# Performance work log

Measured on AMD Instinct MI355X. Metric: run time of the kernel, lower is better.

The kernel has to match this reference:

```python
import math
import jax, jax.numpy as jnp
from jax import lax
import numpy as np

SCORE_THR = 0.5
IOU_THR = 0.7
MIN_SIZE = 1.0
BBOX_CLIP = math.log(1000.0 / 16.0)

FEAT_SIZES = [100, 50, 25, 13, 7]
STRIDES = [8, 16, 32, 64, 128]
RATIOS = (0.5, 1.0, 2.0)
C = 256
A = 3
N = 2


def _make_priors(fs, stride):
    base = stride * 4.0
    ys, xs = np.meshgrid(np.arange(fs), np.arange(fs), indexing='ij')
    cx = (xs + 0.5) * stride
    cy = (ys + 0.5) * stride
    pri = []
    for r in RATIOS:
        w = base / np.sqrt(r)
        h = base * np.sqrt(r)
        pri.append(np.stack([cx - w / 2, cy - h / 2, cx + w / 2, cy + h / 2], axis=-1))
    pri = np.stack(pri, axis=2)  # (fs, fs, A, 4): H,W,A order matches permute/reshape
    return jnp.asarray(pri.reshape(-1, 4), dtype=jnp.float32)


def setup_inputs():
    key = jax.random.key(0)
    ks = jax.random.split(key, 8)
    inp = {}
    for i, fs in enumerate(FEAT_SIZES):
        inp[f'fmap{i}'] = jax.random.normal(jax.random.fold_in(ks[0], i), (N, C, fs, fs), dtype=jnp.float32)
        inp[f'priors{i}'] = _make_priors(fs, STRIDES[i])
    sc = 0.02
    inp['conv_w'] = jax.random.normal(ks[1], (C, C, 3, 3), jnp.float32) * sc
    inp['conv_b'] = jnp.zeros((C,), jnp.float32)
    inp['log_w'] = jax.random.normal(ks[2], (A, C, 1, 1), jnp.float32) * sc
    inp['log_b'] = jnp.zeros((A,), jnp.float32)
    inp['reg_w'] = jax.random.normal(ks[3], (A * 4, C, 1, 1), jnp.float32) * sc
    inp['reg_b'] = jnp.zeros((A * 4,), jnp.float32)
    inp['imsizes'] = jnp.full((N, 2), 800, dtype=jnp.int32)  # (h, w) per image
    inp['lvtop'] = 500
    inp['imtop'] = 100
    return inp


def _conv(x, w, b, pad):
    y = lax.conv_general_dilated(x, w, (1, 1), pad, dimension_numbers=('NCHW', 'OIHW', 'NCHW'))
    return y + b[None, :, None, None]


def _decode(reg, pri):
    pw = pri[..., 2] - pri[..., 0]
    ph = pri[..., 3] - pri[..., 1]
    pcx = pri[..., 0] + 0.5 * pw
    pcy = pri[..., 1] + 0.5 * ph
    dx, dy = reg[..., 0], reg[..., 1]
    dw = jnp.minimum(reg[..., 2], BBOX_CLIP)
    dh = jnp.minimum(reg[..., 3], BBOX_CLIP)
    cx = dx * pw + pcx
    cy = dy * ph + pcy
    w = jnp.exp(dw) * pw
    h = jnp.exp(dh) * ph
    return jnp.stack([cx - 0.5 * w, cy - 0.5 * h, cx + 0.5 * w, cy + 0.5 * h], axis=-1)


def _head(x, priors, conv_w, conv_b, log_w, log_b, reg_w, reg_b, lvtop):
    n = x.shape[0]
    h = jax.nn.relu(_conv(x, conv_w, conv_b, 'SAME'))
    reg = _conv(h, reg_w, reg_b, 'VALID').transpose(0, 2, 3, 1).reshape(n, -1, 4)
    log = _conv(h, log_w, log_b, 'VALID').transpose(0, 2, 3, 1).reshape(n, -1)
    k = min(lvtop, log.shape[1])
    vals, top = lax.top_k(log, k)                           # (n, k)
    reg = jnp.take_along_axis(reg, top[..., None], axis=1)  # (n, k, 4)
    pri = priors[top]                                       # (n, k, 4)
    return _decode(reg, pri), vals, k


def _box_iou(a, b):
    area_a = (a[:, 2] - a[:, 0]) * (a[:, 3] - a[:, 1])
    area_b = (b[:, 2] - b[:, 0]) * (b[:, 3] - b[:, 1])
    lt = jnp.maximum(a[:, None, :2], b[None, :, :2])
    rb = jnp.minimum(a[:, None, 2:], b[None, :, 2:])
    wh = jnp.clip(rb - lt, 0.0)
    inter = wh[..., 0] * wh[..., 1]
    return inter / (area_a[:, None] + area_b[None, :] - inter + 1e-9)


def _forward(fmaps, priors, conv_w, conv_b, log_w, log_b, reg_w, reg_b, imsizes, lvtop, imtop):
    tups = [_head(x, p, conv_w, conv_b, log_w, log_b, reg_w, reg_b, lvtop)
            for x, p in zip(fmaps, priors)]
    boxes = jnp.concatenate([t[0] for t in tups], axis=1)                 # (n, D, 4)
    obj = jax.nn.sigmoid(jnp.concatenate([t[1] for t in tups], axis=1))   # (n, D)
    lvlen = jnp.asarray([t[2] for t in tups])
    n, D = obj.shape
    boxes = boxes.reshape(-1, 4)
    obj = obj.reshape(-1)
    K = n * D
    imidx = jnp.arange(K) // D
    valid = obj >= SCORE_THR                                # score filter (masked, not nonzero)
    hw = imsizes[imidx].astype(jnp.float32)                 # (K, 2) = (h, w)
    x1 = jnp.clip(boxes[:, 0], 0.0, hw[:, 1])
    y1 = jnp.clip(boxes[:, 1], 0.0, hw[:, 0])
    x2 = jnp.clip(boxes[:, 2], 0.0, hw[:, 1])
    y2 = jnp.clip(boxes[:, 3], 0.0, hw[:, 0])
    boxes = jnp.stack([x1, y1, x2, y2], axis=-1)
    valid &= (x2 - x1 >= MIN_SIZE) & (y2 - y1 >= MIN_SIZE)  # remove_small
    lvidx = jnp.searchsorted(jnp.cumsum(lvlen), jnp.arange(K) % D, side='right')
    groups = imidx * 10 + lvidx
    scores = jnp.where(valid, obj, -jnp.inf)
    order = jnp.argsort(-scores)                            # global score order; groups gate suppression
    b, g, v, ii = boxes[order], groups[order], valid[order], imidx[order]
    iou = _box_iou(b, b)                                    # (K, K)
    ar = jnp.arange(K)
    def body(i, keep):
        sup = (iou[i] > IOU_THR) & (g == g[i]) & (ar > i)
        return jnp.where(keep[i], keep & ~sup, keep)
    keep = lax.fori_loop(0, K, body, v)                     # greedy batched NMS
    def select(i):
        m = keep & (ii == i)
        sel = jnp.argsort(~m)[:imtop]                       # stable: kept boxes in score order
        val = m[sel]
        bx = jnp.where(val[:, None], b[sel], 0.0)
        ix = jnp.where(val, i, -1)
        return bx, ix
    bx, ix = jax.vmap(select)(jnp.arange(n))
    return bx.reshape(n * imtop, 4), ix.reshape(n * imtop)


def reference(fmap0, fmap1, fmap2, fmap3, fmap4, priors0, priors1, priors2, priors3, priors4,
              conv_w, conv_b, log_w, log_b, reg_w, reg_b, imsizes, lvtop, imtop):
    return _forward([fmap0, fmap1, fmap2, fmap3, fmap4],
                    [priors0, priors1, priors2, priors3, priors4],
                    conv_w, conv_b, log_w, log_b, reg_w, reg_b, imsizes, lvtop, imtop)
```

## Files before the change

### kernel.cpp

```cpp
#include <hip/hip_runtime.h>
#include <math.h>


#define N_IMG 2
#define C_CH  256
#define D_PER 2147
#define K_TOT 4294
#define K_PAD 8192

__constant__ int c_Ml[5]     = {30000, 7500, 1875, 507, 147};
__constant__ int c_kl[5]     = {500, 500, 500, 500, 147};
__constant__ int c_lvoff[5]  = {0, 500, 1000, 1500, 2000};
__constant__ int c_logoff[5] = {0, 60000, 75000, 78750, 79764};
__constant__ int c_regoff[5] = {0, 240000, 300000, 315000, 319056};
__constant__ int c_fs[5]     = {100, 50, 25, 13, 7};
__constant__ int c_npt[5]    = {13, 7, 4, 2, 1};
__constant__ int c_E[5]      = {10000, 2500, 625, 169, 49};
__constant__ int c_cumbl[6]  = {0, 1352, 1744, 1872, 1904, 1912};
__constant__ int c_hcum[6]   = {0, 157, 197, 207, 210, 211};
__constant__ size_t c_hoff[5] = {0, 5120000, 6400000, 6720000, 6806528};

__global__ void transpose_w_kernel(const float* __restrict__ w,
                                   double* __restrict__ wT2) {
  int i = blockIdx.x * 256 + threadIdx.x;
  if (i >= 589824) return;
  int q = i % 4608;
  int slab = i / 4608;
  int cobi = slab >> 5, ch = slab & 31;
  int ci = q / 576;
  int rem = q % 576;
  int tap = rem / 64, co = rem & 63;
  wT2[i] = (double)w[(size_t)(cobi * 64 + co) * 2304 + (ch * 8 + ci) * 9 + tap];
}

template <typename T>
__global__ __launch_bounds__(256) void conv_fused_kernel(
    const float* __restrict__ x0, const float* __restrict__ x1,
    const float* __restrict__ x2, const float* __restrict__ x3,
    const float* __restrict__ x4, const double* __restrict__ wT2,
    const float* __restrict__ bias, T* __restrict__ h) {
  __shared__ double s_in[8][120];
  __shared__ double s_w[4608];
  int tid = threadIdx.x;
  int bid = blockIdx.x;
  int l = 0;
  while (bid >= c_cumbl[l + 1]) ++l;
  int r = bid - c_cumbl[l];
  int fs = c_fs[l], npt = c_npt[l];
  int tiles = npt * npt;
  int tile = r % tiles;
  int cn = r / tiles;
  int cobi = cn & 3, n = cn >> 2;
  int ptx = tile % npt, pty = tile / npt;
  int px0 = ptx * 8, py0 = pty * 8;
  int E = fs * fs;
  const float* xl;
  switch (l) {
    case 0: xl = x0; break;
    case 1: xl = x1; break;
    case 2: xl = x2; break;
    case 3: xl = x3; break;
    default: xl = x4; break;
  }
  const float* xn = xl + (size_t)n * C_CH * E;
  T* hl = h + c_hoff[l];

  int tpx = tid & 15, tco = tid >> 4;
  int prow = tpx >> 1, pcol0 = (tpx & 1) * 4;

  double acc[4][4];
#pragma unroll
  for (int i = 0; i < 4; i++)
#pragma unroll
    for (int j = 0; j < 4; j++) acc[i][j] = 0.0;

  for (int ch = 0; ch < 32; ++ch) {
    for (int idx = tid; idx < 800; idx += 256) {
      int ci = idx / 100, rr2 = idx % 100;
      int hy = rr2 / 10, hx = rr2 % 10;
      int gy = py0 - 1 + hy, gx = px0 - 1 + hx;
      float v = 0.f;
      if (gy >= 0 && gy < fs && gx >= 0 && gx < fs)
        v = xn[(size_t)(ch * 8 + ci) * E + gy * fs + gx];
      s_in[ci][hy * 12 + hx] = (double)v;
    }
    {
      const double2* src =
          (const double2*)(wT2 + (size_t)(cobi * 32 + ch) * 4608);
      double2* dst = (double2*)s_w;
#pragma unroll
      for (int k = 0; k < 9; k++) {
        int idx = tid + k * 256;
        if (idx < 2304) dst[idx] = src[idx];
      }
    }
    __syncthreads();
#pragma unroll
    for (int ci = 0; ci < 8; ++ci) {
      const double* inp = &s_in[ci][0];
      const double* wpb = &s_w[ci * 576];
#pragma unroll
      for (int ky = 0; ky < 3; ++ky) {
        const double* ip = inp + (prow + ky) * 12 + pcol0;
        double2 a0 = *(const double2*)ip;
        double2 a1 = *(const double2*)(ip + 2);
        double2 a2 = *(const double2*)(ip + 4);
        double d6[6];
        d6[0] = a0.x; d6[1] = a0.y; d6[2] = a1.x;
        d6[3] = a1.y; d6[4] = a2.x; d6[5] = a2.y;
#pragma unroll
        for (int kx = 0; kx < 3; ++kx) {
          const double* wp = wpb + (ky * 3 + kx) * 64 + tco * 4;
          double2 wA = *(const double2*)wp;
          double2 wB = *(const double2*)(wp + 2);
          double w0 = wA.x, w1 = wA.y, w2 = wB.x, w3 = wB.y;
#pragma unroll
          for (int pj = 0; pj < 4; pj++) {
            double iv = d6[pj + kx];
            acc[0][pj] = fma(w0, iv, acc[0][pj]);
            acc[1][pj] = fma(w1, iv, acc[1][pj]);
            acc[2][pj] = fma(w2, iv, acc[2][pj]);
            acc[3][pj] = fma(w3, iv, acc[3][pj]);
          }
        }
      }
    }
    __syncthreads();
  }

  int gy = py0 + prow;
  if (gy < fs) {
#pragma unroll
    for (int coi = 0; coi < 4; ++coi) {
      int co = cobi * 64 + tco * 4 + coi;
      double bb = (double)bias[co];
#pragma unroll
      for (int pj = 0; pj < 4; pj++) {
        int gx = px0 + pcol0 + pj;
        if (gx < fs) {
          double v = acc[coi][pj] + bb;
          hl[((size_t)n * C_CH + co) * E + gy * fs + gx] = (T)fmax(v, 0.0);
        }
      }
    }
  }
}

template <typename T>
__global__ __launch_bounds__(256) void heads_fused_kernel(
    const T* __restrict__ h, const float* __restrict__ logw,
    const float* __restrict__ logb, const float* __restrict__ regw,
    const float* __restrict__ regb, double* __restrict__ logits,
    double* __restrict__ regs) {
  __shared__ float s_wh[256][16];
  __shared__ double s_red[4][15][64];
  int tid = threadIdx.x;
  int n = blockIdx.y;
  int cidx = blockIdx.x;
  int l = 0;
  while (cidx >= c_hcum[l + 1]) ++l;
  int chunk = cidx - c_hcum[l];
  int E = c_E[l];
  int px0 = chunk * 64;
  const T* hl = h + c_hoff[l];
  double* logits_l = logits + c_logoff[l];
  double* regs_l = regs + c_regoff[l];

  for (int idx = tid; idx < 4096; idx += 256) {
    int c = idx >> 4, j = idx & 15;
    float v = 0.f;
    if (j < 3) v = logw[j * 256 + c];
    else if (j < 15) v = regw[(j - 3) * 256 + c];
    s_wh[c][j] = v;
  }
  __syncthreads();

  int p = tid & 63, c4 = tid >> 6;
  int pix = px0 + p;
  bool act = pix < E;
  double acc[15];
#pragma unroll
  for (int j = 0; j < 15; j++) acc[j] = 0.0;
  if (act) {
    const T* hp = hl + ((size_t)n * C_CH + c4 * 64) * E + pix;
    for (int cc = 0; cc < 64; ++cc) {
      double hv = (double)hp[(size_t)cc * E];
      const float* wr = &s_wh[c4 * 64 + cc][0];
#pragma unroll
      for (int j = 0; j < 15; j++)
        acc[j] = fma((double)wr[j], hv, acc[j]);
    }
  }
#pragma unroll
  for (int j = 0; j < 15; j++) s_red[c4][j][p] = acc[j];
  __syncthreads();
  if (act) {
    int M = E * 3;
    for (int j = c4; j < 15; j += 4) {
      double v = s_red[0][j][p] + s_red[1][j][p] + s_red[2][j][p] +
                 s_red[3][j][p];
      if (j < 3) {
        logits_l[(size_t)n * M + pix * 3 + j] = v + (double)logb[j];
      } else {
        int rj = j - 3, a = rj >> 2, coord = rj & 3;
        regs_l[((size_t)n * M + pix * 3 + a) * 4 + coord] =
            v + (double)regb[rj];
      }
    }
  }
}

__device__ __forceinline__ unsigned long long d2key(double v) {
  unsigned long long ub = (unsigned long long)__double_as_longlong(v);
  return (ub >> 63) ? ~ub : (ub | 0x8000000000000000ull);
}

#define TK_CH 30
__global__ __launch_bounds__(1024) void topk_kernel(
    const double* __restrict__ logits, int* __restrict__ cand_anchor) {
  int bid = blockIdx.x;
  int n = bid / 5, l = bid % 5;
  int M = c_Ml[l], k = c_kl[l];
  const double* lg = logits + c_logoff[l] + (size_t)n * M;
  int tid = threadIdx.x;
  __shared__ int histw[16][256];
  __shared__ int hist[256];
  __shared__ unsigned long long s_prefix;
  __shared__ int s_r;
  if (tid == 0) { s_prefix = 0ull; s_r = k; }

  int chunk = (M + 1023) >> 10;
  int i0 = tid * chunk, i1 = min(M, i0 + chunk);
  int cnt = i1 - i0;
  if (cnt < 0) cnt = 0;
  unsigned long long kv[TK_CH];
#pragma unroll
  for (int q = 0; q < TK_CH; q++)
    if (q < cnt) kv[q] = d2key(lg[i0 + q]);
  int wid = tid >> 6;
  __syncthreads();

  for (int pass = 0; pass < 8; ++pass) {
    int shift = 56 - pass * 8;
    for (int i = tid; i < 4096; i += 1024) ((int*)histw)[i] = 0;
    __syncthreads();
    unsigned long long pfx = s_prefix;
    int rr = s_r;
#pragma unroll
    for (int q = 0; q < TK_CH; q++) {
      if (q < cnt) {
        unsigned long long u = kv[q];
        if (pass == 0 || (u >> (shift + 8)) == pfx)
          atomicAdd(&histw[wid][(int)((u >> shift) & 255ull)], 1);
      }
    }
    __syncthreads();
    if (tid < 256) {
      int s = 0;
#pragma unroll
      for (int w = 0; w < 16; w++) s += histw[w][tid];
      hist[tid] = s;
    }
    __syncthreads();
    if (tid == 0) {
      int s = 0, beta = 0;
      for (int b = 255; b >= 0; --b) {
        if (s + hist[b] >= rr) { beta = b; break; }
        s += hist[b];
      }
      s_prefix = (pfx << 8) | (unsigned long long)beta;
      s_r = rr - s;
    }
    __syncthreads();
  }
  unsigned long long T = s_prefix;
  int need = s_r;
  int cgt = 0, ceq = 0;
#pragma unroll
  for (int q = 0; q < TK_CH; q++) {
    if (q < cnt) {
      cgt += (kv[q] > T);
      ceq += (kv[q] == T);
    }
  }
  __shared__ int sgt[1024], seq[1024];
  sgt[tid] = cgt;
  seq[tid] = ceq;
  __syncthreads();
  for (int o = 1; o < 1024; o <<= 1) {
    int a = (tid >= o) ? sgt[tid - o] : 0;
    int b2 = (tid >= o) ? seq[tid - o] : 0;
    __syncthreads();
    sgt[tid] += a;
    seq[tid] += b2;
    __syncthreads();
  }
  int gt_total = sgt[1023];
  int pg = sgt[tid] - cgt, pe = seq[tid] - ceq;
  int base = n * D_PER + c_lvoff[l];
#pragma unroll
  for (int q = 0; q < TK_CH; q++) {
    if (q < cnt) {
      unsigned long long u = kv[q];
      if (u > T) {
        cand_anchor[base + (pg++)] = i0 + q;
      } else if (u == T) {
        if (pe < need) cand_anchor[base + gt_total + pe] = i0 + q;
        pe++;
      }
    }
  }
}

__global__ __launch_bounds__(256) void decode_kernel(
    const int* __restrict__ cand_anchor, const double* __restrict__ logits,
    const double* __restrict__ regs, const float* __restrict__ p0,
    const float* __restrict__ p1, const float* __restrict__ p2,
    const float* __restrict__ p3, const float* __restrict__ p4,
    const int* __restrict__ imsizes, double* __restrict__ cand_score,
    double* __restrict__ cand_box, int* __restrict__ cand_group,
    int* __restrict__ cand_valid) {
  int s = blockIdx.x * 256 + threadIdx.x;
  if (s >= K_TOT) return;
  int n = s / D_PER;
  int rr = s % D_PER;
  int l = (rr < 2000) ? (rr / 500) : 4;
  int aidx = cand_anchor[s];
  int M = c_Ml[l];
  const float* pp;
  switch (l) {
    case 0: pp = p0; break;
    case 1: pp = p1; break;
    case 2: pp = p2; break;
    case 3: pp = p3; break;
    default: pp = p4; break;
  }
  double lv = logits[c_logoff[l] + (size_t)n * M + aidx];
  double obj = 1.0 / (1.0 + exp(-lv));
  const double* rp = regs + c_regoff[l] + ((size_t)n * M + aidx) * 4;
  const float* pr = pp + (size_t)aidx * 4;
  double px1 = pr[0], py1 = pr[1], px2 = pr[2], py2 = pr[3];
  double pw = px2 - px1, ph = py2 - py1;
  double pcx = px1 + 0.5 * pw, pcy = py1 + 0.5 * ph;
  const double BCLIP = 4.1351665567423560;
  double dx = rp[0], dy = rp[1];
  double dw = fmin(rp[2], BCLIP), dh = fmin(rp[3], BCLIP);
  double cx = dx * pw + pcx, cy = dy * ph + pcy;
  double w = exp(dw) * pw, hh = exp(dh) * ph;
  double x1 = cx - 0.5 * w, y1 = cy - 0.5 * hh;
  double x2 = cx + 0.5 * w, y2 = cy + 0.5 * hh;
  double imh = (double)imsizes[n * 2 + 0], imw = (double)imsizes[n * 2 + 1];
  x1 = fmin(fmax(x1, 0.0), imw);
  x2 = fmin(fmax(x2, 0.0), imw);
  y1 = fmin(fmax(y1, 0.0), imh);
  y2 = fmin(fmax(y2, 0.0), imh);
  bool valid = (obj >= 0.5) && ((x2 - x1) >= 1.0) && ((y2 - y1) >= 1.0);
  cand_box[(size_t)s * 4 + 0] = x1;
  cand_box[(size_t)s * 4 + 1] = y1;
  cand_box[(size_t)s * 4 + 2] = x2;
  cand_box[(size_t)s * 4 + 3] = y2;
  cand_score[s] = valid ? obj : -(double)INFINITY;
  cand_group[s] = n * 5 + l;
  cand_valid[s] = valid ? 1 : 0;
}

__global__ __launch_bounds__(1024) void sort_kernel(
    const double* __restrict__ cand_score, int* __restrict__ order) {
  __shared__ unsigned long long key[K_PAD];
  int tid = threadIdx.x;
  for (int i = tid; i < K_PAD; i += 1024) {
    unsigned long long kk = 0ull;
    if (i < K_TOT) {
      unsigned long long u = d2key(cand_score[i]);
      kk = (u & ~0x1FFFull) | (unsigned long long)i;
    }
    key[i] = kk;
  }
  __syncthreads();
  for (int k = 2; k <= K_PAD; k <<= 1) {
    for (int j = k >> 1; j > 0; j >>= 1) {
      for (int i = tid; i < K_PAD; i += 1024) {
        int ixj = i ^ j;
        if (ixj > i) {
          unsigned long long a = key[i], b = key[ixj];
          bool sw = ((i & k) == 0) ? (a < b) : (a > b);
          if (sw) { key[i] = b; key[ixj] = a; }
        }
      }
      __syncthreads();
    }
  }
  for (int i = tid; i < K_TOT; i += 1024)
    order[i] = (int)(key[i] & 0x1FFFull);
}

__global__ __launch_bounds__(256) void gather_kernel(
    const int* __restrict__ order, const double* __restrict__ cand_box,
    const int* __restrict__ cand_group, const int* __restrict__ cand_valid,
    double* __restrict__ box_s, int* __restrict__ grp_s,
    int* __restrict__ img_s, int* __restrict__ valid_s,
    int* __restrict__ keep_s) {
  int i = blockIdx.x * 256 + threadIdx.x;
  if (i >= K_TOT) return;
  int s = order[i];
#pragma unroll
  for (int q = 0; q < 4; q++)
    box_s[(size_t)i * 4 + q] = cand_box[(size_t)s * 4 + q];
  int g = cand_group[s];
  grp_s[i] = g;
  img_s[i] = g / 5;
  valid_s[i] = cand_valid[s];
  keep_s[i] = 0;
}

#define MAXM 512
__global__ __launch_bounds__(256) void nms_kernel(
    const double* __restrict__ box_s, const int* __restrict__ grp_s,
    const int* __restrict__ valid_s, int* __restrict__ keep_s) {
  int g = blockIdx.x;
  int tid = threadIdx.x;
  __shared__ int cnt[256];
  __shared__ int mem[MAXM];
  __shared__ double bx[MAXM][4];
  __shared__ unsigned long long mask[MAXM][8];
  const int chunk = (K_TOT + 255) / 256;
  int i0 = tid * chunk, i1 = min(K_TOT, i0 + chunk);
  int c = 0;
  for (int i = i0; i < i1; ++i) c += (grp_s[i] == g && valid_s[i]);
  cnt[tid] = c;
  __syncthreads();
  for (int o = 1; o < 256; o <<= 1) {
    int v = (tid >= o) ? cnt[tid - o] : 0;
    __syncthreads();
    cnt[tid] += v;
    __syncthreads();
  }
  int off = cnt[tid] - c;
  int m = cnt[255];
  for (int i = i0; i < i1; ++i)
    if (grp_s[i] == g && valid_s[i]) mem[off++] = i;
  __syncthreads();
  for (int t = tid; t < m; t += 256) {
    int i = mem[t];
#pragma unroll
    for (int q = 0; q < 4; q++) bx[t][q] = box_s[(size_t)i * 4 + q];
  }
  __syncthreads();
  for (int i = tid; i < m; i += 256) {
    unsigned long long row[8] = {0, 0, 0, 0, 0, 0, 0, 0};
    double ax1 = bx[i][0], ay1 = bx[i][1], ax2 = bx[i][2], ay2 = bx[i][3];
    double areaA = (ax2 - ax1) * (ay2 - ay1);
    for (int j = i + 1; j < m; ++j) {
      double bx1 = bx[j][0], by1 = bx[j][1], bx2 = bx[j][2], by2 = bx[j][3];
      double areaB = (bx2 - bx1) * (by2 - by1);
      double lx = fmax(ax1, bx1), ly = fmax(ay1, by1);
      double rx = fmin(ax2, bx2), ry = fmin(ay2, by2);
      double iw = fmax(rx - lx, 0.0), ih = fmax(ry - ly, 0.0);
      double inter = iw * ih;
      double iou = inter / (areaA + areaB - inter + 1e-9);
      if (iou > 0.7) row[j >> 6] |= (1ull << (j & 63));
    }
#pragma unroll
    for (int w2 = 0; w2 < 8; ++w2) mask[i][w2] = row[w2];
  }
  __syncthreads();
  if (tid == 0) {
    unsigned long long remv[8] = {0, 0, 0, 0, 0, 0, 0, 0};
    for (int i = 0; i < m; ++i) {
      if (!((remv[i >> 6] >> (i & 63)) & 1ull)) {
        keep_s[mem[i]] = 1;
#pragma unroll
        for (int w2 = 0; w2 < 8; ++w2) remv[w2] |= mask[i][w2];
      }
    }
  }
}

__global__ __launch_bounds__(256) void select_kernel(
    const double* __restrict__ box_s, const int* __restrict__ img_s,
    const int* __restrict__ keep_s, float* __restrict__ out) {
  int n = blockIdx.x;
  int tid = threadIdx.x;
  __shared__ int cnt[256];
  const int chunk = (K_TOT + 255) / 256;
  int i0 = tid * chunk, i1 = min(K_TOT, i0 + chunk);
  int c = 0;
  for (int i = i0; i < i1; ++i) c += (keep_s[i] && img_s[i] == n);
  cnt[tid] = c;
  __syncthreads();
  for (int o = 1; o < 256; o <<= 1) {
    int v = (tid >= o) ? cnt[tid - o] : 0;
    __syncthreads();
    cnt[tid] += v;
    __syncthreads();
  }
  int pos = cnt[tid] - c;
  int total = cnt[255];
  for (int i = i0; i < i1; ++i) {
    if (keep_s[i] && img_s[i] == n) {
      if (pos < 100) {
#pragma unroll
        for (int q = 0; q < 4; q++)
          out[(n * 100 + pos) * 4 + q] = (float)box_s[(size_t)i * 4 + q];
        out[800 + n * 100 + pos] = (float)n;
      }
      pos++;
    }
  }
  for (int p = total + tid; p < 100; p += 256) {
#pragma unroll
    for (int q = 0; q < 4; q++) out[(n * 100 + p) * 4 + q] = 0.0f;
    out[800 + n * 100 + p] = -1.0f;
  }
}

extern "C" void kernel_launch(void* const* d_in, const int* in_sizes, int n_in,
                              void* d_out, int out_size, void* d_ws,
                              size_t ws_size, hipStream_t stream) {
  (void)in_sizes; (void)n_in; (void)out_size;
  const float* fmap[5];
  const float* priors[5];
  for (int l = 0; l < 5; l++) {
    fmap[l] = (const float*)d_in[2 * l];
    priors[l] = (const float*)d_in[2 * l + 1];
  }
  const float* conv_w = (const float*)d_in[10];
  const float* conv_b = (const float*)d_in[11];
  const float* log_w = (const float*)d_in[12];
  const float* log_b = (const float*)d_in[13];
  const float* reg_w = (const float*)d_in[14];
  const float* reg_b = (const float*)d_in[15];
  const int* imsizes = (const int*)d_in[16];
  float* out = (float*)d_out;

  bool f64h = ws_size >= (size_t)66000000;

  char* base = (char*)d_ws;
  size_t off = 0;
  auto alloc = [&](size_t bytes) -> void* {
    off = (off + 255) & ~(size_t)255;
    void* p = base + off;
    off += bytes;
    return p;
  };
  double* wT2 = (double*)alloc(589824ull * 8);
  void* hraw = alloc(6831616ull * (f64h ? 8 : 4));
  double* logits = (double*)alloc(80058ull * 8);
  double* regs = (double*)alloc(320232ull * 8);
  int* cand_anchor = (int*)alloc(K_TOT * 4);
  double* cand_score = (double*)alloc(K_TOT * 8);
  double* cand_box = (double*)alloc((size_t)K_TOT * 4 * 8);
  int* cand_group = (int*)alloc(K_TOT * 4);
  int* cand_valid = (int*)alloc(K_TOT * 4);
  int* order = (int*)alloc(K_TOT * 4);
  double* box_s = (double*)alloc((size_t)K_TOT * 4 * 8);
  int* grp_s = (int*)alloc(K_TOT * 4);
  int* img_s = (int*)alloc(K_TOT * 4);
  int* valid_s = (int*)alloc(K_TOT * 4);
  int* keep_s = (int*)alloc(K_TOT * 4);

  transpose_w_kernel<<<2304, 256, 0, stream>>>(conv_w, wT2);

  if (f64h) {
    conv_fused_kernel<double><<<1912, 256, 0, stream>>>(
        fmap[0], fmap[1], fmap[2], fmap[3], fmap[4], wT2, conv_b,
        (double*)hraw);
    heads_fused_kernel<double><<<dim3(211, 2), 256, 0, stream>>>(
        (double*)hraw, log_w, log_b, reg_w, reg_b, logits, regs);
  } else {
    conv_fused_kernel<float><<<1912, 256, 0, stream>>>(
        fmap[0], fmap[1], fmap[2], fmap[3], fmap[4], wT2, conv_b,
        (float*)hraw);
    heads_fused_kernel<float><<<dim3(211, 2), 256, 0, stream>>>(
        (float*)hraw, log_w, log_b, reg_w, reg_b, logits, regs);
  }
  topk_kernel<<<10, 1024, 0, stream>>>(logits, cand_anchor);
  decode_kernel<<<(K_TOT + 255) / 256, 256, 0, stream>>>(
      cand_anchor, logits, regs, priors[0], priors[1], priors[2], priors[3],
      priors[4], imsizes, cand_score, cand_box, cand_group, cand_valid);
  sort_kernel<<<1, 1024, 0, stream>>>(cand_score, order);
  gather_kernel<<<(K_TOT + 255) / 256, 256, 0, stream>>>(
      order, cand_box, cand_group, cand_valid, box_s, grp_s, img_s, valid_s,
      keep_s);
  nms_kernel<<<10, 256, 0, stream>>>(box_s, grp_s, valid_s, keep_s);
  select_kernel<<<2, 256, 0, stream>>>(box_s, img_s, keep_s, out);
}
```

Before: 1.239 ms.

## Halve conv channel chunk, precompute halo indices, and remap block order

The fp64 3x3 conv now stages 4 input channels per iteration instead of 8, which halves shared memory (s_w 2304 doubles, s_in 480) so more blocks can be resident per CU. The halo load addresses are computed once before the channel loop rather than recomputed with divisions every iteration. Block IDs are permuted with a stride of 239 so neighbouring launched blocks come from different regions of the work list, likely to spread them across XCDs. The trade-off is twice as many loop iterations and barriers, with less work per barrier.

```diff
diff --git a/kernel.cpp b/kernel.cpp
--- a/kernel.cpp
+++ b/kernel.cpp
@@ -7,6 +7,8 @@
 #define D_PER 2147
 #define K_TOT 4294
 #define K_PAD 8192
+#define CONV_BLOCKS 1912
+#define CPX 239
 
 __constant__ int c_Ml[5]     = {30000, 7500, 1875, 507, 147};
 __constant__ int c_kl[5]     = {500, 500, 500, 500, 147};
@@ -24,13 +26,14 @@
                                    double* __restrict__ wT2) {
   int i = blockIdx.x * 256 + threadIdx.x;
   if (i >= 589824) return;
-  int q = i % 4608;
-  int slab = i / 4608;
-  int cobi = slab >> 5, ch = slab & 31;
+  int q = i % 2304;
+  int slab = i / 2304;
+  int cobi = slab >> 6, ch = slab & 63;
   int ci = q / 576;
   int rem = q % 576;
   int tap = rem / 64, co = rem & 63;
-  wT2[i] = (double)w[(size_t)(cobi * 64 + co) * 2304 + (ch * 8 + ci) * 9 + tap];
+  wT2[i] =
+      (double)w[(size_t)(cobi * 64 + co) * 2304 + (ch * 4 + ci) * 9 + tap];
 }
 
 template <typename T>
@@ -39,10 +42,10 @@
     const float* __restrict__ x2, const float* __restrict__ x3,
     const float* __restrict__ x4, const double* __restrict__ wT2,
     const float* __restrict__ bias, T* __restrict__ h) {
-  __shared__ double s_in[8][120];
-  __shared__ double s_w[4608];
+  __shared__ double s_in[4 * 120];
+  __shared__ double s_w[2304];
   int tid = threadIdx.x;
-  int bid = blockIdx.x;
+  int bid = (blockIdx.x & 7) * CPX + (blockIdx.x >> 3);
   int l = 0;
   while (bid >= c_cumbl[l + 1]) ++l;
   int r = bid - c_cumbl[l];
@@ -68,36 +71,52 @@
   int tpx = tid & 15, tco = tid >> 4;
   int prow = tpx >> 1, pcol0 = (tpx & 1) * 4;
 
-  double acc[4][4];
-#pragma unroll
-  for (int i = 0; i < 4; i++)
-#pragma unroll
-    for (int j = 0; j < 4; j++) acc[i][j] = 0.0;
-
-  for (int ch = 0; ch < 32; ++ch) {
-    for (int idx = tid; idx < 800; idx += 256) {
+  int in_dst[2], in_src[2];
+#pragma unroll
+  for (int it = 0; it < 2; ++it) {
+    int idx = tid + it * 256;
+    in_dst[it] = -1;
+    in_src[it] = -1;
+    if (idx < 400) {
       int ci = idx / 100, rr2 = idx % 100;
       int hy = rr2 / 10, hx = rr2 % 10;
       int gy = py0 - 1 + hy, gx = px0 - 1 + hx;
-      float v = 0.f;
+      in_dst[it] = ci * 120 + hy * 12 + hx;
       if (gy >= 0 && gy < fs && gx >= 0 && gx < fs)
-        v = xn[(size_t)(ch * 8 + ci) * E + gy * fs + gx];
-      s_in[ci][hy * 12 + hx] = (double)v;
+        in_src[it] = ci * E + gy * fs + gx;
+    }
+  }
+
+  double acc[4][4];
+#pragma unroll
+  for (int i = 0; i < 4; i++)
+#pragma unroll
+    for (int j = 0; j < 4; j++) acc[i][j] = 0.0;
+
+  const double2* wsrc0 = (const double2*)(wT2 + (size_t)cobi * 64 * 2304);
+
+  for (int ch = 0; ch < 64; ++ch) {
+    const float* xc = xn + (size_t)ch * 4 * E;
+#pragma unroll
+    for (int it = 0; it < 2; ++it) {
+      if (in_dst[it] >= 0) {
+        float v = (in_src[it] >= 0) ? xc[in_src[it]] : 0.f;
+        s_in[in_dst[it]] = (double)v;
+      }
     }
     {
-      const double2* src =
-          (const double2*)(wT2 + (size_t)(cobi * 32 + ch) * 4608);
+      const double2* src = wsrc0 + (size_t)ch * 1152;
       double2* dst = (double2*)s_w;
 #pragma unroll
-      for (int k = 0; k < 9; k++) {
+      for (int k = 0; k < 5; k++) {
         int idx = tid + k * 256;
-        if (idx < 2304) dst[idx] = src[idx];
-      }
-    }
-    __syncthreads();
-#pragma unroll
-    for (int ci = 0; ci < 8; ++ci) {
-      const double* inp = &s_in[ci][0];
+        if (idx < 1152) dst[idx] = src[idx];
+      }
+    }
+    __syncthreads();
+#pragma unroll
+    for (int ci = 0; ci < 4; ++ci) {
+      const double* inp = &s_in[ci * 120];
       const double* wpb = &s_w[ci * 576];
 #pragma unroll
       for (int ky = 0; ky < 3; ++ky) {
@@ -562,13 +581,13 @@
   transpose_w_kernel<<<2304, 256, 0, stream>>>(conv_w, wT2);
 
   if (f64h) {
-    conv_fused_kernel<double><<<1912, 256, 0, stream>>>(
+    conv_fused_kernel<double><<<CONV_BLOCKS, 256, 0, stream>>>(
         fmap[0], fmap[1], fmap[2], fmap[3], fmap[4], wT2, conv_b,
         (double*)hraw);
     heads_fused_kernel<double><<<dim3(211, 2), 256, 0, stream>>>(
         (double*)hraw, log_w, log_b, reg_w, reg_b, logits, regs);
   } else {
-    conv_fused_kernel<float><<<1912, 256, 0, stream>>>(
+    conv_fused_kernel<float><<<CONV_BLOCKS, 256, 0, stream>>>(
         fmap[0], fmap[1], fmap[2], fmap[3], fmap[4], wT2, conv_b,
         (float*)hraw);
     heads_fused_kernel<float><<<dim3(211, 2), 256, 0, stream>>>(
```

After: 1.199 ms. 3.2% less time.
